# Performance work log

Hardware: AMD Instinct MI355X
Metric: run time of the kernel (lower is better)

Reference implementation:

```python
import jax, jax.numpy as jnp
import numpy as np

B, M, N, E = 64, 100, 6400, 102400   # graphs, nodes/graph, total nodes, edges
H, D, EMB, IMG, NC = 4, 512, 768, 1024, 2
HD = H * D
EPS = 1e-5


def _bn2(x, g, b, m, v):
    # BatchNorm1d eval mode on [B, C]
    return (x - m) / jnp.sqrt(v + EPS) * g + b


def _bn3(x, g, b, m, v):
    # BatchNorm1d eval mode on [B, C, L] -> channel dim is axis 1 (node index)
    return (x - m[None, :, None]) / jnp.sqrt(v + EPS)[None, :, None] * g[None, :, None] + b[None, :, None]


def _gat(feat, src, dst, W, al, ar, bias):
    # DGL GATConv (eval: feat_drop is identity). feat: [N, F_in]
    h = (feat @ W.T).reshape(-1, H, D)                 # [N, H, D]
    el = (h * al[None]).sum(-1)                         # [N, H]
    er = (h * ar[None]).sum(-1)                         # [N, H]
    e = jax.nn.leaky_relu(el[src] + er[dst], negative_slope=0.2)  # [E, H]
    mx = jax.ops.segment_max(e, dst, num_segments=N)
    a = jnp.exp(e - mx[dst])
    s = jax.ops.segment_sum(a, dst, num_segments=N)
    alpha = a / s[dst]                                  # edge softmax over incoming edges
    out = jax.ops.segment_sum(h[src] * alpha[:, :, None], dst, num_segments=N)  # [N, H, D]
    return out + bias.reshape(1, H, D)


def setup_inputs() -> dict:
    key = jax.random.key(0)
    ks = iter(jax.random.split(key, 80))
    n = lambda *s: jax.random.normal(next(ks), s, dtype=jnp.float32)

    def bn(c):
        return (1.0 + 0.1 * n(c), 0.1 * n(c), 0.1 * n(c),
                0.5 + jax.random.uniform(next(ks), (c,), dtype=jnp.float32))

    s = 0.02
    inp = {}
    inp['img_embedding'] = n(B, IMG)
    inp['func_text_embedding'] = n(B, EMB)
    inp['unix_emb'] = n(N, EMB)
    inp['pos_emb'] = jax.random.uniform(next(ks), (N, 4), dtype=jnp.float32)
    inp['src'] = jax.random.randint(next(ks), (E,), 0, N)
    inp['dst'] = jax.random.randint(next(ks), (E,), 0, N)
    inp['gat1_W'] = n(HD, EMB) * s; inp['gat1_al'] = n(H, D) * 0.1; inp['gat1_ar'] = n(H, D) * 0.1; inp['gat1_b'] = jnp.zeros(HD)
    inp['gat2_W'] = n(HD, HD) * s; inp['gat2_al'] = n(H, D) * 0.1; inp['gat2_ar'] = n(H, D) * 0.1; inp['gat2_b'] = jnp.zeros(HD)
    inp['fc_W'] = n(D, HD) * s; inp['fc_b'] = jnp.zeros(D)
    inp['hidden_W'] = n(8, D, D) * s; inp['hidden_b'] = jnp.zeros((8, D))
    inp['bn_text_g'], inp['bn_text_b'], inp['bn_text_m'], inp['bn_text_v'] = bn(EMB)
    inp['fc_text_W'] = n(D, EMB) * s; inp['fc_text_b'] = jnp.zeros(D)
    inp['swin_g'], inp['swin_b'], inp['swin_m'], inp['swin_v'] = bn(IMG)
    inp['swinfc_W'] = n(D, IMG) * s; inp['swinfc_b'] = jnp.zeros(D)
    inp['bngat_g'], inp['bngat_b'], inp['bngat_m'], inp['bngat_v'] = bn(M)
    inp['fc_gat_W'] = n(480, D) * s; inp['fc_gat_b'] = jnp.zeros(480)
    inp['bnbb_g'], inp['bnbb_b'], inp['bnbb_m'], inp['bnbb_v'] = bn(M)
    inp['fc_bbox_W'] = n(32, 4) * s; inp['fc_bbox_b'] = jnp.zeros(32)
    inp['fbn_g'], inp['fbn_b'], inp['fbn_m'], inp['fbn_v'] = bn(3 * D)
    inp['final_W'] = n(NC, 3 * D) * s; inp['final_b'] = jnp.zeros(NC)
    return inp


def reference(img_embedding, func_text_embedding, unix_emb, pos_emb, src, dst,
              gat1_W, gat1_al, gat1_ar, gat1_b, gat2_W, gat2_al, gat2_ar, gat2_b,
              fc_W, fc_b, hidden_W, hidden_b,
              bn_text_g, bn_text_b, bn_text_m, bn_text_v, fc_text_W, fc_text_b,
              swin_g, swin_b, swin_m, swin_v, swinfc_W, swinfc_b,
              bngat_g, bngat_b, bngat_m, bngat_v, fc_gat_W, fc_gat_b,
              bnbb_g, bnbb_b, bnbb_m, bnbb_v, fc_bbox_W, fc_bbox_b,
              fbn_g, fbn_b, fbn_m, fbn_v, final_W, final_b):
    # image branch
    x = jax.nn.elu(_bn2(img_embedding, swin_g, swin_b, swin_m, swin_v) @ swinfc_W.T + swinfc_b)
    # text branch
    ft = jax.nn.elu(_bn2(func_text_embedding, bn_text_g, bn_text_b, bn_text_m, bn_text_v) @ fc_text_W.T + fc_text_b)
    # graph branch: two stacked GATConv layers (dropout is identity in eval)
    h = _gat(unix_emb, src, dst, gat1_W, gat1_al, gat1_ar, gat1_b).reshape(N, HD)
    h = _gat(h, src, dst, gat2_W, gat2_al, gat2_ar, gat2_b).reshape(N, HD)
    h = jax.nn.elu(h @ fc_W.T + fc_b)
    for i in range(8):
        h = jax.nn.elu(h @ hidden_W[i].T + hidden_b[i])
    # unbatch + pad to max_node=100 -> pure reshape (all graphs have exactly M nodes)
    h_i = h.reshape(B, M, D)
    pos_i = pos_emb.reshape(B, M, 4)
    h_i = jax.nn.elu(_bn3(h_i, bngat_g, bngat_b, bngat_m, bngat_v) @ fc_gat_W.T + fc_gat_b)      # [B, M, 480]
    pos_i = jax.nn.elu(_bn3(pos_i, bnbb_g, bnbb_b, bnbb_m, bnbb_v) @ fc_bbox_W.T + fc_bbox_b)    # [B, M, 32]
    h_feature = jnp.concatenate([h_i, pos_i], axis=2).mean(axis=1)                                # [B, 512]
    all_feats = jnp.concatenate([x, h_feature, ft], axis=1)                                       # [B, 1536]
    return _bn2(all_feats, fbn_g, fbn_b, fbn_m, fbn_v) @ final_W.T + final_b
```

## Files before the change

kernel.cpp:

```cpp
#include <hip/hip_runtime.h>
#include <math.h>

#define Bg   64
#define Mg   100
#define Ng   6400
#define Eg   102400
#define Hh   4
#define Dd   512
#define HDd  2048
#define EMBd 768
#define IMGd 1024
#define EPSc 1e-5f

typedef __bf16 bf16x8 __attribute__((ext_vector_type(8)));
typedef float  f32x4  __attribute__((ext_vector_type(4)));
typedef unsigned short us8v __attribute__((ext_vector_type(8)));

__device__ __forceinline__ float eluf(float x) { return x > 0.f ? x : expm1f(x); }

__device__ __forceinline__ unsigned short f2bf(float x) {
    unsigned int u = __builtin_bit_cast(unsigned int, x);
    u += 0x7FFFu + ((u >> 16) & 1u);
    return (unsigned short)(u >> 16);
}
__device__ __forceinline__ float bf2f(unsigned short s) {
    return __builtin_bit_cast(float, ((unsigned int)s) << 16);
}

__device__ __forceinline__ void gld16(const void* g, void* l) {
    __builtin_amdgcn_global_load_lds(
        (const __attribute__((address_space(1))) void*)g,
        (__attribute__((address_space(3))) void*)l, 16, 0, 0);
}

__global__ __launch_bounds__(256)
void gemm_bf16(const unsigned short* __restrict__ A,
               const unsigned short* __restrict__ W,
               const float* __restrict__ bias, void* __restrict__ C,
               int M, int N, int K, int act, int outbf)
{
    __shared__ __align__(16) unsigned short As[128 * 32];
    __shared__ __align__(16) unsigned short Bs[128 * 32];
    const int tid  = threadIdx.x;
    const int lane = tid & 63, wid = tid >> 6;
    const int bm = blockIdx.y * 128, bn = blockIdx.x * 128;
    const int wm = (wid >> 1) * 64, wn = (wid & 1) * 64;
    const int lrow = lane >> 2;
    const int lcol = (lane & 3) << 3;

    f32x4 acc[4][4] = {};

    const int ra = wid * 32;
    const unsigned short* gA0 = A + (size_t)(bm + ra + lrow) * K + lcol;
    const unsigned short* gA1 = A + (size_t)(bm + ra + 16 + lrow) * K + lcol;
    int rb0 = bn + ra + lrow;       if (rb0 >= N) rb0 = N - 1;
    int rb1 = bn + ra + 16 + lrow;  if (rb1 >= N) rb1 = N - 1;
    const unsigned short* gB0 = W + (size_t)rb0 * K + lcol;
    const unsigned short* gB1 = W + (size_t)rb1 * K + lcol;
    unsigned short* lA0 = &As[(ra)      * 32];
    unsigned short* lA1 = &As[(ra + 16) * 32];
    unsigned short* lB0 = &Bs[(ra)      * 32];
    unsigned short* lB1 = &Bs[(ra + 16) * 32];

    const int frow = lane & 15;
    const int quad = (lane >> 4) << 3;

    for (int k0 = 0; k0 < K; k0 += 32) {
        gld16(gA0 + k0, lA0);
        gld16(gA1 + k0, lA1);
        gld16(gB0 + k0, lB0);
        gld16(gB1 + k0, lB1);
        __syncthreads();
        bf16x8 af[4], bfr[4];
#pragma unroll
        for (int i = 0; i < 4; ++i)
            af[i]  = *(const bf16x8*)&As[(wm + i * 16 + frow) * 32 + quad];
#pragma unroll
        for (int i = 0; i < 4; ++i)
            bfr[i] = *(const bf16x8*)&Bs[(wn + i * 16 + frow) * 32 + quad];
#pragma unroll
        for (int mi = 0; mi < 4; ++mi)
#pragma unroll
            for (int ni = 0; ni < 4; ++ni)
                acc[mi][ni] = __builtin_amdgcn_mfma_f32_16x16x32_bf16(
                    af[mi], bfr[ni], acc[mi][ni], 0, 0, 0);
        __syncthreads();
    }

    const int crow0 = bm + wm + ((lane >> 4) << 2);
    const int ccol0 = bn + wn + (lane & 15);
#pragma unroll
    for (int mi = 0; mi < 4; ++mi) {
#pragma unroll
        for (int ni = 0; ni < 4; ++ni) {
            int col = ccol0 + ni * 16;
            if (col >= N) continue;
            float bv = bias ? bias[col] : 0.f;
#pragma unroll
            for (int r = 0; r < 4; ++r) {
                int row = crow0 + mi * 16 + r;
                float v = acc[mi][ni][r] + bv;
                if (act) v = eluf(v);
                if (outbf) ((unsigned short*)C)[(size_t)row * N + col] = f2bf(v);
                else       ((float*)C)[(size_t)row * N + col] = v;
            }
        }
    }
}

__global__ __launch_bounds__(256)
void gemm_t64b(const unsigned short* __restrict__ A,
               const unsigned short* __restrict__ W,
               const float* __restrict__ bias, void* __restrict__ C,
               int M, int N, int K, int act, int outbf)
{
    __shared__ __align__(16) unsigned short As[2 * 64 * 32];
    __shared__ __align__(16) unsigned short Bs[2 * 64 * 32];
    const int tid  = threadIdx.x;
    const int lane = tid & 63, wid = tid >> 6;
    const int bm = blockIdx.y * 64, bn = blockIdx.x * 64;
    const int wm = (wid >> 1) * 32, wn = (wid & 1) * 32;
    const int lrow = lane >> 2;
    const int lcol = (lane & 3) << 3;

    f32x4 acc[2][2] = {};

    const int r0 = wid * 16;
    const unsigned short* gA = A + (size_t)(bm + r0 + lrow) * K + lcol;
    int rb = bn + r0 + lrow; if (rb >= N) rb = N - 1;
    const unsigned short* gB = W + (size_t)rb * K + lcol;
    unsigned short* lA0 = &As[r0 * 32];
    unsigned short* lA1 = &As[2048 + r0 * 32];
    unsigned short* lB0 = &Bs[r0 * 32];
    unsigned short* lB1 = &Bs[2048 + r0 * 32];

    const int frow = lane & 15;
    const int quad = (lane >> 4) << 3;

    for (int k0 = 0; k0 < K; k0 += 64) {
        gld16(gA + k0,      lA0);
        gld16(gA + k0 + 32, lA1);
        gld16(gB + k0,      lB0);
        gld16(gB + k0 + 32, lB1);
        __syncthreads();
#pragma unroll
        for (int ks = 0; ks < 2; ++ks) {
            bf16x8 af0 = *(const bf16x8*)&As[ks * 2048 + (wm + frow) * 32 + quad];
            bf16x8 af1 = *(const bf16x8*)&As[ks * 2048 + (wm + 16 + frow) * 32 + quad];
            bf16x8 bf0 = *(const bf16x8*)&Bs[ks * 2048 + (wn + frow) * 32 + quad];
            bf16x8 bf1 = *(const bf16x8*)&Bs[ks * 2048 + (wn + 16 + frow) * 32 + quad];
            acc[0][0] = __builtin_amdgcn_mfma_f32_16x16x32_bf16(af0, bf0, acc[0][0], 0, 0, 0);
            acc[0][1] = __builtin_amdgcn_mfma_f32_16x16x32_bf16(af0, bf1, acc[0][1], 0, 0, 0);
            acc[1][0] = __builtin_amdgcn_mfma_f32_16x16x32_bf16(af1, bf0, acc[1][0], 0, 0, 0);
            acc[1][1] = __builtin_amdgcn_mfma_f32_16x16x32_bf16(af1, bf1, acc[1][1], 0, 0, 0);
        }
        __syncthreads();
    }

    const int crow0 = bm + wm + ((lane >> 4) << 2);
    const int ccol0 = bn + wn + (lane & 15);
#pragma unroll
    for (int mi = 0; mi < 2; ++mi) {
#pragma unroll
        for (int ni = 0; ni < 2; ++ni) {
            int col = ccol0 + ni * 16;
            if (col >= N) continue;
            float bv = bias ? bias[col] : 0.f;
#pragma unroll
            for (int r = 0; r < 4; ++r) {
                int row = crow0 + mi * 16 + r;
                float v = acc[mi][ni][r] + bv;
                if (act) v = eluf(v);
                if (outbf) ((unsigned short*)C)[(size_t)row * N + col] = f2bf(v);
                else       ((float*)C)[(size_t)row * N + col] = v;
            }
        }
    }
}

__global__ __launch_bounds__(256)
void gemm_t64b_fcgat(const unsigned short* __restrict__ A,
                     const unsigned short* __restrict__ W,
                     const float* __restrict__ bfg, const float* __restrict__ wsum,
                     const float* __restrict__ bng, const float* __restrict__ bnb,
                     const float* __restrict__ bnm, const float* __restrict__ bnv,
                     unsigned short* __restrict__ Eout, int M, int N, int K)
{
    __shared__ __align__(16) unsigned short As[2 * 64 * 32];
    __shared__ __align__(16) unsigned short Bs[2 * 64 * 32];
    const int tid  = threadIdx.x;
    const int lane = tid & 63, wid = tid >> 6;
    const int bm = blockIdx.y * 64, bn = blockIdx.x * 64;
    const int wm = (wid >> 1) * 32, wn = (wid & 1) * 32;
    const int lrow = lane >> 2;
    const int lcol = (lane & 3) << 3;

    f32x4 acc[2][2] = {};

    const int r0 = wid * 16;
    const unsigned short* gA = A + (size_t)(bm + r0 + lrow) * K + lcol;
    int rb = bn + r0 + lrow; if (rb >= N) rb = N - 1;
    const unsigned short* gB = W + (size_t)rb * K + lcol;
    unsigned short* lA0 = &As[r0 * 32];
    unsigned short* lA1 = &As[2048 + r0 * 32];
    unsigned short* lB0 = &Bs[r0 * 32];
    unsigned short* lB1 = &Bs[2048 + r0 * 32];

    const int frow = lane & 15;
    const int quad = (lane >> 4) << 3;

    for (int k0 = 0; k0 < K; k0 += 64) {
        gld16(gA + k0,      lA0);
        gld16(gA + k0 + 32, lA1);
        gld16(gB + k0,      lB0);
        gld16(gB + k0 + 32, lB1);
        __syncthreads();
#pragma unroll
        for (int ks = 0; ks < 2; ++ks) {
            bf16x8 af0 = *(const bf16x8*)&As[ks * 2048 + (wm + frow) * 32 + quad];
            bf16x8 af1 = *(const bf16x8*)&As[ks * 2048 + (wm + 16 + frow) * 32 + quad];
            bf16x8 bf0 = *(const bf16x8*)&Bs[ks * 2048 + (wn + frow) * 32 + quad];
            bf16x8 bf1 = *(const bf16x8*)&Bs[ks * 2048 + (wn + 16 + frow) * 32 + quad];
            acc[0][0] = __builtin_amdgcn_mfma_f32_16x16x32_bf16(af0, bf0, acc[0][0], 0, 0, 0);
            acc[0][1] = __builtin_amdgcn_mfma_f32_16x16x32_bf16(af0, bf1, acc[0][1], 0, 0, 0);
            acc[1][0] = __builtin_amdgcn_mfma_f32_16x16x32_bf16(af1, bf0, acc[1][0], 0, 0, 0);
            acc[1][1] = __builtin_amdgcn_mfma_f32_16x16x32_bf16(af1, bf1, acc[1][1], 0, 0, 0);
        }
        __syncthreads();
    }

    const int crow0 = bm + wm + ((lane >> 4) << 2);
    const int ccol0 = bn + wn + (lane & 15);
#pragma unroll
    for (int mi = 0; mi < 2; ++mi) {
#pragma unroll
        for (int r = 0; r < 4; ++r) {
            int row = crow0 + mi * 16 + r;
            int p = row % Mg;
            float sc = rsqrtf(bnv[p] + EPSc) * bng[p];
            float sh = bnb[p] - bnm[p] * sc;
#pragma unroll
            for (int ni = 0; ni < 2; ++ni) {
                int col = ccol0 + ni * 16;
                if (col < N) {
                    float v = sc * acc[mi][ni][r] + sh * wsum[col] + bfg[col];
                    Eout[(size_t)row * N + col] = f2bf(eluf(v));
                }
            }
        }
    }
}

__global__ __launch_bounds__(256)
void wsum_kernel(const float* __restrict__ W, float* __restrict__ s)
{
    int row = (blockIdx.x << 2) + (threadIdx.x >> 6);
    int lane = threadIdx.x & 63;
    if (row >= 480) return;
    const float* p = W + (size_t)row * Dd;
    float a = 0.f;
    for (int k = lane; k < Dd; k += 64) a += p[k];
#pragma unroll
    for (int o = 32; o > 0; o >>= 1) a += __shfl_down(a, o, 64);
    if (lane == 0) s[row] = a;
}

__global__ __launch_bounds__(256)
void gemm_nt(const float* __restrict__ A, const float* __restrict__ W,
             const float* __restrict__ bias, float* __restrict__ C,
             int M, int N, int K, int act)
{
    __shared__ float As[16 * 68];
    __shared__ float Ws[16 * 68];
    const int tid = threadIdx.x;
    const int tx = tid & 15, ty = tid >> 4;
    const int bm = blockIdx.y * 64, bn = blockIdx.x * 64;
    const int lrow = tid >> 2;
    const int lk4  = (tid & 3) << 2;
    const int arow = bm + lrow;
    const int wrow = bn + lrow;
    const float* Aptr = A + (size_t)arow * K + lk4;
    const float* Wptr = W + (size_t)wrow * K + lk4;
    float acc[4][4] = {{0.f,0.f,0.f,0.f},{0.f,0.f,0.f,0.f},{0.f,0.f,0.f,0.f},{0.f,0.f,0.f,0.f}};

    for (int k0 = 0; k0 < K; k0 += 16) {
        float4 av = make_float4(0.f,0.f,0.f,0.f);
        float4 wv = make_float4(0.f,0.f,0.f,0.f);
        if (arow < M) av = *(const float4*)(Aptr + k0);
        if (wrow < N) wv = *(const float4*)(Wptr + k0);
        As[(lk4+0)*68 + lrow] = av.x;
        As[(lk4+1)*68 + lrow] = av.y;
        As[(lk4+2)*68 + lrow] = av.z;
        As[(lk4+3)*68 + lrow] = av.w;
        Ws[(lk4+0)*68 + lrow] = wv.x;
        Ws[(lk4+1)*68 + lrow] = wv.y;
        Ws[(lk4+2)*68 + lrow] = wv.z;
        Ws[(lk4+3)*68 + lrow] = wv.w;
        __syncthreads();
#pragma unroll
        for (int kk = 0; kk < 16; ++kk) {
            float4 a = *(const float4*)&As[kk*68 + (ty<<2)];
            float4 w = *(const float4*)&Ws[kk*68 + (tx<<2)];
            acc[0][0] += a.x*w.x; acc[0][1] += a.x*w.y; acc[0][2] += a.x*w.z; acc[0][3] += a.x*w.w;
            acc[1][0] += a.y*w.x; acc[1][1] += a.y*w.y; acc[1][2] += a.y*w.z; acc[1][3] += a.y*w.w;
            acc[2][0] += a.z*w.x; acc[2][1] += a.z*w.y; acc[2][2] += a.z*w.z; acc[2][3] += a.z*w.w;
            acc[3][0] += a.w*w.x; acc[3][1] += a.w*w.y; acc[3][2] += a.w*w.z; acc[3][3] += a.w*w.w;
        }
        __syncthreads();
    }

#pragma unroll
    for (int i = 0; i < 4; ++i) {
        int row = bm + (ty<<2) + i;
        int col = bn + (tx<<2);
        if (row < M && col < N) {
            float4 v;
            v.x = acc[i][0]; v.y = acc[i][1]; v.z = acc[i][2]; v.w = acc[i][3];
            if (bias) { v.x += bias[col]; v.y += bias[col+1]; v.z += bias[col+2]; v.w += bias[col+3]; }
            if (act == 1) { v.x = eluf(v.x); v.y = eluf(v.y); v.z = eluf(v.z); v.w = eluf(v.w); }
            *(float4*)(C + (size_t)row * N + col) = v;
        }
    }
}

struct CvtPack {
    const float* s[6];
    unsigned short* d[6];
    int n4[6];
};

__global__ void cvt_all(CvtPack p, int total4)
{
    int i = blockIdx.x * 256 + threadIdx.x;
    if (i >= total4) return;
#pragma unroll
    for (int k = 0; k < 6; ++k) {
        if (i < p.n4[k]) {
            float4 v = ((const float4*)p.s[k])[i];
            ushort4 o;
            o.x = f2bf(v.x); o.y = f2bf(v.y); o.z = f2bf(v.z); o.w = f2bf(v.w);
            ((ushort4*)p.d[k])[i] = o;
            return;
        }
        i -= p.n4[k];
    }
}

__global__ void bn_col(const float* __restrict__ x, const float* __restrict__ g,
                       const float* __restrict__ b, const float* __restrict__ m,
                       const float* __restrict__ v, float* __restrict__ y,
                       int rows, int cols)
{
    int i = blockIdx.x * 256 + threadIdx.x;
    if (i >= rows * cols) return;
    int c = i % cols;
    float inv = rsqrtf(v[c] + EPSc);
    y[i] = (x[i] - m[c]) * inv * g[c] + b[c];
}

__global__ void zero_i32(int* __restrict__ p, int n)
{
    int i = blockIdx.x * 256 + threadIdx.x;
    if (i < n) p[i] = 0;
}

__global__ void count_dst(const int* __restrict__ dst, int* __restrict__ counts, int E)
{
    int i = blockIdx.x * 256 + threadIdx.x;
    if (i < E) atomicAdd(&counts[dst[i]], 1);
}

__global__ __launch_bounds__(1024)
void scan_excl(const int* __restrict__ counts, int* __restrict__ offs,
               int* __restrict__ cursor, int n)
{
    const int T = 7;
    int tid = threadIdx.x;
    int base = tid * T;
    int v[T];
    int tot = 0;
#pragma unroll
    for (int j = 0; j < T; ++j) {
        int i = base + j;
        v[j] = (i < n) ? counts[i] : 0;
        tot += v[j];
    }
    int lane = tid & 63, w = tid >> 6;
    int incl = tot;
#pragma unroll
    for (int o = 1; o < 64; o <<= 1) {
        int t = __shfl_up(incl, o, 64);
        if (lane >= o) incl += t;
    }
    __shared__ int wtot[16];
    __shared__ int wbase[16];
    if (lane == 63) wtot[w] = incl;
    __syncthreads();
    if (tid == 0) {
        int s = 0;
        for (int i = 0; i < 16; ++i) { wbase[i] = s; s += wtot[i]; }
    }
    __syncthreads();
    int ex = wbase[w] + incl - tot;
#pragma unroll
    for (int j = 0; j < T; ++j) {
        int i = base + j;
        if (i < n) { offs[i] = ex; cursor[i] = ex; }
        ex += v[j];
    }
    if (tid == 1023) offs[n] = ex;
}

__global__ void scatter_edges(const int* __restrict__ dst, int* __restrict__ cursor,
                              int* __restrict__ eid, int E)
{
    int i = blockIdx.x * 256 + threadIdx.x;
    if (i < E) {
        int p = atomicAdd(&cursor[dst[i]], 1);
        eid[p] = i;
    }
}

__global__ __launch_bounds__(256)
void elr_kernel(const unsigned short* __restrict__ Hm, const float* __restrict__ al,
                const float* __restrict__ ar, float* __restrict__ el,
                float* __restrict__ er)
{
    int wid = threadIdx.x >> 6, lane = threadIdx.x & 63;
    int g = (blockIdx.x << 2) + wid;
    int n = g >> 2, h = g & 3;
    const unsigned short* hp = Hm + ((size_t)n << 11) + (h << 9) + (lane << 3);
    const float* alp = al + (h << 9) + (lane << 3);
    const float* arp = ar + (h << 9) + (lane << 3);
    ushort4 x0 = *(const ushort4*)hp;
    ushort4 x1 = *(const ushort4*)(hp + 4);
    float4 l0 = *(const float4*)alp, l1 = *(const float4*)(alp + 4);
    float4 r0 = *(const float4*)arp, r1 = *(const float4*)(arp + 4);
    float a0 = bf2f(x0.x), a1 = bf2f(x0.y), a2 = bf2f(x0.z), a3 = bf2f(x0.w);
    float a4 = bf2f(x1.x), a5 = bf2f(x1.y), a6 = bf2f(x1.z), a7 = bf2f(x1.w);
    float se = a0*l0.x + a1*l0.y + a2*l0.z + a3*l0.w + a4*l1.x + a5*l1.y + a6*l1.z + a7*l1.w;
    float sr = a0*r0.x + a1*r0.y + a2*r0.z + a3*r0.w + a4*r1.x + a5*r1.y + a6*r1.z + a7*r1.w;
#pragma unroll
    for (int o = 32; o > 0; o >>= 1) {
        se += __shfl_down(se, o, 64);
        sr += __shfl_down(sr, o, 64);
    }
    if (lane == 0) { el[g] = se; er[g] = sr; }
}

__global__ __launch_bounds__(256)
void gat_agg(const unsigned short* __restrict__ Hm, const float* __restrict__ el,
             const float* __restrict__ er, const int* __restrict__ src,
             const int* __restrict__ offs, const int* __restrict__ eid,
             const float* __restrict__ bias, unsigned short* __restrict__ out)
{
    int n = blockIdx.x;
    int tid = threadIdx.x;
    int beg = offs[n], end = offs[n + 1];
    int deg = end - beg;
    const int d0 = tid << 3;
    const int h  = tid >> 6;

    if (deg == 0) {
#pragma unroll
        for (int j = 0; j < 8; ++j)
            out[((size_t)n << 11) + d0 + j] = f2bf(bias[d0 + j]);
        return;
    }

    __shared__ float m_sh[4], s_sh[4], al_sh[4];
    __shared__ int   src_sh[128];
    __shared__ float logit_sh[512];
    __shared__ float w_sh[512];

    if (tid < 4) { m_sh[tid] = -INFINITY; s_sh[tid] = 0.f; }
    float acc[8] = {0.f,0.f,0.f,0.f,0.f,0.f,0.f,0.f};
    __syncthreads();

    for (int c0 = 0; c0 < deg; c0 += 128) {
        int cnt = min(128, deg - c0);
        for (int i = tid; i < cnt; i += 256) src_sh[i] = src[eid[beg + c0 + i]];
        __syncthreads();
        for (int idx = tid; idx < (cnt << 2); idx += 256) {
            int i = idx >> 2, hh = idx & 3;
            float x = el[(src_sh[i] << 2) + hh] + er[(n << 2) + hh];
            logit_sh[idx] = x > 0.f ? x : 0.2f * x;
        }
        __syncthreads();
        if (tid < 4) {
            float cm = -INFINITY;
            for (int i = 0; i < cnt; ++i) cm = fmaxf(cm, logit_sh[(i << 2) + tid]);
            float mn = fmaxf(m_sh[tid], cm);
            al_sh[tid] = expf(m_sh[tid] - mn);
            m_sh[tid] = mn;
        }
        __syncthreads();
        for (int idx = tid; idx < (cnt << 2); idx += 256)
            w_sh[idx] = expf(logit_sh[idx] - m_sh[idx & 3]);
        __syncthreads();
        if (tid < 4) {
            float cs = 0.f;
            for (int i = 0; i < cnt; ++i) cs += w_sh[(i << 2) + tid];
            s_sh[tid] = s_sh[tid] * al_sh[tid] + cs;
        }
        float rsc = al_sh[h];
#pragma unroll
        for (int j = 0; j < 8; ++j) acc[j] *= rsc;
        for (int i = 0; i < cnt; ++i) {
            const unsigned short* hp = Hm + ((size_t)src_sh[i] << 11) + d0;
            us8v a = *(const us8v*)hp;
            float w0 = w_sh[(i << 2) + h];
#pragma unroll
            for (int j = 0; j < 8; ++j) acc[j] += w0 * bf2f(a[j]);
        }
        __syncthreads();
    }

    float is = 1.f / s_sh[h];
#pragma unroll
    for (int j = 0; j < 8; ++j)
        out[((size_t)n << 11) + d0 + j] = f2bf(acc[j] * is + bias[d0 + j]);
}

__global__ __launch_bounds__(256)
void mean_kernel(const unsigned short* __restrict__ hg, const float* __restrict__ pos,
                 const float* __restrict__ bg, const float* __restrict__ bb_,
                 const float* __restrict__ bm_, const float* __restrict__ bv_,
                 const float* __restrict__ W, const float* __restrict__ bias,
                 float* __restrict__ hf)
{
    int bb = blockIdx.x;
    int tid = threadIdx.x;
    int c0 = tid, c1 = tid + 256;
    const unsigned short* hb = hg + (size_t)bb * Mg * 480;
    float s0 = 0.f, s1 = 0.f;
    for (int m = 0; m < Mg; ++m) {
        s0 += bf2f(hb[m * 480 + c0]);
        if (c1 < 480) s1 += bf2f(hb[m * 480 + c1]);
    }
    if (c1 >= 480) {
        int o = c1 - 480;
        float w0 = W[(o << 2) + 0], w1 = W[(o << 2) + 1];
        float w2 = W[(o << 2) + 2], w3 = W[(o << 2) + 3];
        float bo = bias[o];
        const float* pp = pos + (size_t)bb * Mg * 4;
        s1 = 0.f;
        for (int m = 0; m < Mg; ++m) {
            float sc = rsqrtf(bv_[m] + EPSc) * bg[m];
            float sh = bb_[m] - bm_[m] * sc;
            float a = bo + (pp[m*4+0]*sc+sh)*w0 + (pp[m*4+1]*sc+sh)*w1
                         + (pp[m*4+2]*sc+sh)*w2 + (pp[m*4+3]*sc+sh)*w3;
            s1 += eluf(a);
        }
    }
    hf[bb * 512 + c0] = s0 * 0.01f;
    hf[bb * 512 + c1] = s1 * 0.01f;
}

__global__ __launch_bounds__(256)
void final_kernel(const float* __restrict__ x, const float* __restrict__ hf,
                  const float* __restrict__ ft, const float* __restrict__ g,
                  const float* __restrict__ b, const float* __restrict__ m,
                  const float* __restrict__ v, const float* __restrict__ W,
                  const float* __restrict__ bias, float* __restrict__ out)
{
    int bb = blockIdx.x;
    int tid = threadIdx.x;
    float a0 = 0.f, a1 = 0.f;
    for (int c = tid; c < 1536; c += 256) {
        float xv = (c < 512) ? x[bb * 512 + c]
                 : (c < 1024) ? hf[bb * 512 + (c - 512)]
                              : ft[bb * 512 + (c - 1024)];
        float z = (xv - m[c]) * rsqrtf(v[c] + EPSc) * g[c] + b[c];
        a0 += z * W[c];
        a1 += z * W[1536 + c];
    }
    __shared__ float r0[256], r1[256];
    r0[tid] = a0; r1[tid] = a1;
    __syncthreads();
    for (int o = 128; o > 0; o >>= 1) {
        if (tid < o) { r0[tid] += r0[tid + o]; r1[tid] += r1[tid + o]; }
        __syncthreads();
    }
    if (tid == 0) {
        out[bb * 2 + 0] = r0[0] + bias[0];
        out[bb * 2 + 1] = r1[0] + bias[1];
    }
}

extern "C" void kernel_launch(void* const* d_in, const int* in_sizes, int n_in,
                              void* d_out, int out_size, void* d_ws, size_t ws_size,
                              hipStream_t stream)
{
    (void)in_sizes; (void)n_in; (void)out_size; (void)ws_size;

    const float* img   = (const float*)d_in[0];
    const float* ftxt  = (const float*)d_in[1];
    const float* unixe = (const float*)d_in[2];
    const float* pos   = (const float*)d_in[3];
    const int*   src   = (const int*)  d_in[4];
    const int*   dst   = (const int*)  d_in[5];
    const float* g1W   = (const float*)d_in[6];
    const float* g1al  = (const float*)d_in[7];
    const float* g1ar  = (const float*)d_in[8];
    const float* g1b   = (const float*)d_in[9];
    const float* g2W   = (const float*)d_in[10];
    const float* g2al  = (const float*)d_in[11];
    const float* g2ar  = (const float*)d_in[12];
    const float* g2b   = (const float*)d_in[13];
    const float* fcW   = (const float*)d_in[14];
    const float* fcb   = (const float*)d_in[15];
    const float* hidW  = (const float*)d_in[16];
    const float* hidb  = (const float*)d_in[17];
    const float* btg   = (const float*)d_in[18];
    const float* btb   = (const float*)d_in[19];
    const float* btm   = (const float*)d_in[20];
    const float* btv   = (const float*)d_in[21];
    const float* ftW   = (const float*)d_in[22];
    const float* ftbi  = (const float*)d_in[23];
    const float* swg   = (const float*)d_in[24];
    const float* swb   = (const float*)d_in[25];
    const float* swm   = (const float*)d_in[26];
    const float* swv   = (const float*)d_in[27];
    const float* swW   = (const float*)d_in[28];
    const float* swbi  = (const float*)d_in[29];
    const float* bgg   = (const float*)d_in[30];
    const float* bgb   = (const float*)d_in[31];
    const float* bgm   = (const float*)d_in[32];
    const float* bgv   = (const float*)d_in[33];
    const float* fgW   = (const float*)d_in[34];
    const float* fgb   = (const float*)d_in[35];
    const float* bbgp  = (const float*)d_in[36];
    const float* bbbp  = (const float*)d_in[37];
    const float* bbmp  = (const float*)d_in[38];
    const float* bbvp  = (const float*)d_in[39];
    const float* fbW   = (const float*)d_in[40];
    const float* fbb   = (const float*)d_in[41];
    const float* fng   = (const float*)d_in[42];
    const float* fnb   = (const float*)d_in[43];
    const float* fnm   = (const float*)d_in[44];
    const float* fnv   = (const float*)d_in[45];
    const float* fiW   = (const float*)d_in[46];
    const float* fib   = (const float*)d_in[47];
    float* out = (float*)d_out;

    char* p = (char*)d_ws;
    unsigned short* fA  = (unsigned short*)p; p += (size_t)Ng * HDd * 2;
    unsigned short* fB  = (unsigned short*)p; p += (size_t)Ng * HDd * 2;
    unsigned short* fC  = (unsigned short*)p; p += (size_t)Ng * Dd * 2;
    unsigned short* fD  = (unsigned short*)p; p += (size_t)Ng * Dd * 2;
    unsigned short* fE  = (unsigned short*)p; p += (size_t)Ng * 480 * 2;
    float*          el  = (float*)p;          p += (size_t)Ng * Hh * 4;
    float*          er  = (float*)p;          p += (size_t)Ng * Hh * 4;
    float*          xb  = (float*)p;          p += (size_t)Bg * Dd * 4;
    float*          ftb = (float*)p;          p += (size_t)Bg * Dd * 4;
    float*          hf  = (float*)p;          p += (size_t)Bg * Dd * 4;
    float*          ti  = (float*)p;          p += (size_t)Bg * IMGd * 4;
    float*          tt  = (float*)p;          p += (size_t)Bg * EMBd * 4;
    float*          wsm = (float*)p;          p += (size_t)480 * 4;
    unsigned short* ubf = (unsigned short*)p; p += (size_t)Ng * EMBd * 2;
    unsigned short* wg1 = (unsigned short*)p; p += (size_t)HDd * EMBd * 2;
    unsigned short* wg2 = (unsigned short*)p; p += (size_t)HDd * HDd * 2;
    unsigned short* wfc = (unsigned short*)p; p += (size_t)Dd * HDd * 2;
    unsigned short* whid= (unsigned short*)p; p += (size_t)8 * Dd * Dd * 2;
    unsigned short* wfg = (unsigned short*)p; p += (size_t)480 * Dd * 2;
    int* counts = (int*)p; p += (size_t)Ng * 4;
    int* offs   = (int*)p; p += (size_t)(Ng + 1) * 4 + 12;
    int* cursor = (int*)p; p += (size_t)Ng * 4;
    int* eid    = (int*)p; p += (size_t)Eg * 4;

    CvtPack cp;
    cp.s[0] = unixe; cp.d[0] = ubf;  cp.n4[0] = Ng * EMBd / 4;
    cp.s[1] = g1W;   cp.d[1] = wg1;  cp.n4[1] = HDd * EMBd / 4;
    cp.s[2] = g2W;   cp.d[2] = wg2;  cp.n4[2] = HDd * HDd / 4;
    cp.s[3] = fcW;   cp.d[3] = wfc;  cp.n4[3] = Dd * HDd / 4;
    cp.s[4] = hidW;  cp.d[4] = whid; cp.n4[4] = 8 * Dd * Dd / 4;
    cp.s[5] = fgW;   cp.d[5] = wfg;  cp.n4[5] = 480 * Dd / 4;
    int total4 = cp.n4[0] + cp.n4[1] + cp.n4[2] + cp.n4[3] + cp.n4[4] + cp.n4[5];
    cvt_all<<<(total4 + 255)/256, 256, 0, stream>>>(cp, total4);
    wsum_kernel<<<120, 256, 0, stream>>>(fgW, wsm);

    bn_col<<<(Bg*IMGd + 255)/256, 256, 0, stream>>>(img, swg, swb, swm, swv, ti, Bg, IMGd);
    gemm_nt<<<dim3(8, 1), 256, 0, stream>>>(ti, swW, swbi, xb, Bg, Dd, IMGd, 1);
    bn_col<<<(Bg*EMBd + 255)/256, 256, 0, stream>>>(ftxt, btg, btb, btm, btv, tt, Bg, EMBd);
    gemm_nt<<<dim3(8, 1), 256, 0, stream>>>(tt, ftW, ftbi, ftb, Bg, Dd, EMBd, 1);

    zero_i32<<<(Ng + 255)/256, 256, 0, stream>>>(counts, Ng);
    count_dst<<<(Eg + 255)/256, 256, 0, stream>>>(dst, counts, Eg);
    scan_excl<<<1, 1024, 0, stream>>>(counts, offs, cursor, Ng);
    scatter_edges<<<(Eg + 255)/256, 256, 0, stream>>>(dst, cursor, eid, Eg);

    gemm_bf16<<<dim3(HDd/128, Ng/128), 256, 0, stream>>>(ubf, wg1, nullptr, fA, Ng, HDd, EMBd, 0, 1);
    elr_kernel<<<Ng, 256, 0, stream>>>(fA, g1al, g1ar, el, er);
    gat_agg<<<Ng, 256, 0, stream>>>(fA, el, er, src, offs, eid, g1b, fB);

    gemm_bf16<<<dim3(HDd/128, Ng/128), 256, 0, stream>>>(fB, wg2, nullptr, fA, Ng, HDd, HDd, 0, 1);
    elr_kernel<<<Ng, 256, 0, stream>>>(fA, g2al, g2ar, el, er);
    gat_agg<<<Ng, 256, 0, stream>>>(fA, el, er, src, offs, eid, g2b, fB);

    gemm_t64b<<<dim3(Dd/64, Ng/64), 256, 0, stream>>>(fB, wfc, fcb, fC, Ng, Dd, HDd, 1, 1);

    unsigned short* cur = fC; unsigned short* nxt = fD;
    for (int i = 0; i < 8; ++i) {
        gemm_t64b<<<dim3(Dd/64, Ng/64), 256, 0, stream>>>(
            cur, whid + (size_t)i * Dd * Dd, hidb + (size_t)i * Dd, nxt, Ng, Dd, Dd, 1, 1);
        unsigned short* t = cur; cur = nxt; nxt = t;
    }

    gemm_t64b_fcgat<<<dim3(8, Ng/64), 256, 0, stream>>>(
        cur, wfg, fgb, wsm, bgg, bgb, bgm, bgv, fE, Ng, 480, Dd);

    mean_kernel<<<Bg, 256, 0, stream>>>(fE, pos, bbgp, bbbp, bbmp, bbvp, fbW, fbb, hf);

    final_kernel<<<Bg, 256, 0, stream>>>(xb, hf, ftb, fng, fnb, fnm, fnv, fiW, fib, out);
}
```

Baseline: 856.3 us.

## Double-buffer LDS in GEMMs, fuse BN into small GEMMs, prefetch GAT gathers

Converts the three bf16 MFMA GEMM kernels to double-buffered LDS, issuing the next K-tile's global-to-LDS loads before computing the current one. This replaces the load-sync-compute pattern and its two barriers per step with one barrier per iteration. It also folds the eval-mode batchnorm into the A-load of the small fp32 gemm_nt, removing the bn_col kernels and their temporary buffers. The GAT aggregation loop now prefetches the next neighbour's feature row to hide gather latency. Costs are doubled shared memory in the GEMMs, which may reduce occupancy, and extra registers in the aggregation loop.

```diff
diff --git a/kernel.cpp b/kernel.cpp
--- a/kernel.cpp
+++ b/kernel.cpp
@@ -39,8 +39,8 @@
                const float* __restrict__ bias, void* __restrict__ C,
                int M, int N, int K, int act, int outbf)
 {
-    __shared__ __align__(16) unsigned short As[128 * 32];
-    __shared__ __align__(16) unsigned short Bs[128 * 32];
+    __shared__ __align__(16) unsigned short As[2 * 128 * 32];
+    __shared__ __align__(16) unsigned short Bs[2 * 128 * 32];
     const int tid  = threadIdx.x;
     const int lane = tid & 63, wid = tid >> 6;
     const int bm = blockIdx.y * 128, bn = blockIdx.x * 128;
@@ -57,27 +57,35 @@
     int rb1 = bn + ra + 16 + lrow;  if (rb1 >= N) rb1 = N - 1;
     const unsigned short* gB0 = W + (size_t)rb0 * K + lcol;
     const unsigned short* gB1 = W + (size_t)rb1 * K + lcol;
-    unsigned short* lA0 = &As[(ra)      * 32];
-    unsigned short* lA1 = &As[(ra + 16) * 32];
-    unsigned short* lB0 = &Bs[(ra)      * 32];
-    unsigned short* lB1 = &Bs[(ra + 16) * 32];
 
     const int frow = lane & 15;
     const int quad = (lane >> 4) << 3;
-
-    for (int k0 = 0; k0 < K; k0 += 32) {
-        gld16(gA0 + k0, lA0);
-        gld16(gA1 + k0, lA1);
-        gld16(gB0 + k0, lB0);
-        gld16(gB1 + k0, lB1);
-        __syncthreads();
+    const int iters = K >> 5;
+
+    gld16(gA0, &As[(ra)      * 32]);
+    gld16(gA1, &As[(ra + 16) * 32]);
+    gld16(gB0, &Bs[(ra)      * 32]);
+    gld16(gB1, &Bs[(ra + 16) * 32]);
+    __syncthreads();
+
+    int cur = 0;
+    for (int it = 0; it < iters; ++it) {
+        if (it + 1 < iters) {
+            int k1 = (it + 1) << 5;
+            int nb = (cur ^ 1) * 4096;
+            gld16(gA0 + k1, &As[nb + (ra)      * 32]);
+            gld16(gA1 + k1, &As[nb + (ra + 16) * 32]);
+            gld16(gB0 + k1, &Bs[nb + (ra)      * 32]);
+            gld16(gB1 + k1, &Bs[nb + (ra + 16) * 32]);
+        }
+        int cb = cur * 4096;
         bf16x8 af[4], bfr[4];
 #pragma unroll
         for (int i = 0; i < 4; ++i)
-            af[i]  = *(const bf16x8*)&As[(wm + i * 16 + frow) * 32 + quad];
+            af[i]  = *(const bf16x8*)&As[cb + (wm + i * 16 + frow) * 32 + quad];
 #pragma unroll
         for (int i = 0; i < 4; ++i)
-            bfr[i] = *(const bf16x8*)&Bs[(wn + i * 16 + frow) * 32 + quad];
+            bfr[i] = *(const bf16x8*)&Bs[cb + (wn + i * 16 + frow) * 32 + quad];
 #pragma unroll
         for (int mi = 0; mi < 4; ++mi)
 #pragma unroll
@@ -85,6 +93,7 @@
                 acc[mi][ni] = __builtin_amdgcn_mfma_f32_16x16x32_bf16(
                     af[mi], bfr[ni], acc[mi][ni], 0, 0, 0);
         __syncthreads();
+        cur ^= 1;
     }
 
     const int crow0 = bm + wm + ((lane >> 4) << 2);
@@ -114,8 +123,8 @@
                const float* __restrict__ bias, void* __restrict__ C,
                int M, int N, int K, int act, int outbf)
 {
-    __shared__ __align__(16) unsigned short As[2 * 64 * 32];
-    __shared__ __align__(16) unsigned short Bs[2 * 64 * 32];
+    __shared__ __align__(16) unsigned short As[2 * 2 * 64 * 32];
+    __shared__ __align__(16) unsigned short Bs[2 * 2 * 64 * 32];
     const int tid  = threadIdx.x;
     const int lane = tid & 63, wid = tid >> 6;
     const int bm = blockIdx.y * 64, bn = blockIdx.x * 64;
@@ -129,32 +138,41 @@
     const unsigned short* gA = A + (size_t)(bm + r0 + lrow) * K + lcol;
     int rb = bn + r0 + lrow; if (rb >= N) rb = N - 1;
     const unsigned short* gB = W + (size_t)rb * K + lcol;
-    unsigned short* lA0 = &As[r0 * 32];
-    unsigned short* lA1 = &As[2048 + r0 * 32];
-    unsigned short* lB0 = &Bs[r0 * 32];
-    unsigned short* lB1 = &Bs[2048 + r0 * 32];
 
     const int frow = lane & 15;
     const int quad = (lane >> 4) << 3;
-
-    for (int k0 = 0; k0 < K; k0 += 64) {
-        gld16(gA + k0,      lA0);
-        gld16(gA + k0 + 32, lA1);
-        gld16(gB + k0,      lB0);
-        gld16(gB + k0 + 32, lB1);
-        __syncthreads();
+    const int iters = K >> 6;
+
+    gld16(gA,      &As[r0 * 32]);
+    gld16(gA + 32, &As[2048 + r0 * 32]);
+    gld16(gB,      &Bs[r0 * 32]);
+    gld16(gB + 32, &Bs[2048 + r0 * 32]);
+    __syncthreads();
+
+    int cur = 0;
+    for (int it = 0; it < iters; ++it) {
+        if (it + 1 < iters) {
+            int k1 = (it + 1) << 6;
+            int nb = (cur ^ 1) * 4096;
+            gld16(gA + k1,      &As[nb + r0 * 32]);
+            gld16(gA + k1 + 32, &As[nb + 2048 + r0 * 32]);
+            gld16(gB + k1,      &Bs[nb + r0 * 32]);
+            gld16(gB + k1 + 32, &Bs[nb + 2048 + r0 * 32]);
+        }
+        int cb = cur * 4096;
 #pragma unroll
         for (int ks = 0; ks < 2; ++ks) {
-            bf16x8 af0 = *(const bf16x8*)&As[ks * 2048 + (wm + frow) * 32 + quad];
-            bf16x8 af1 = *(const bf16x8*)&As[ks * 2048 + (wm + 16 + frow) * 32 + quad];
-            bf16x8 bf0 = *(const bf16x8*)&Bs[ks * 2048 + (wn + frow) * 32 + quad];
-            bf16x8 bf1 = *(const bf16x8*)&Bs[ks * 2048 + (wn + 16 + frow) * 32 + quad];
+            bf16x8 af0 = *(const bf16x8*)&As[cb + ks * 2048 + (wm + frow) * 32 + quad];
+            bf16x8 af1 = *(const bf16x8*)&As[cb + ks * 2048 + (wm + 16 + frow) * 32 + quad];
+            bf16x8 bf0 = *(const bf16x8*)&Bs[cb + ks * 2048 + (wn + frow) * 32 + quad];
+            bf16x8 bf1 = *(const bf16x8*)&Bs[cb + ks * 2048 + (wn + 16 + frow) * 32 + quad];
             acc[0][0] = __builtin_amdgcn_mfma_f32_16x16x32_bf16(af0, bf0, acc[0][0], 0, 0, 0);
             acc[0][1] = __builtin_amdgcn_mfma_f32_16x16x32_bf16(af0, bf1, acc[0][1], 0, 0, 0);
             acc[1][0] = __builtin_amdgcn_mfma_f32_16x16x32_bf16(af1, bf0, acc[1][0], 0, 0, 0);
             acc[1][1] = __builtin_amdgcn_mfma_f32_16x16x32_bf16(af1, bf1, acc[1][1], 0, 0, 0);
         }
         __syncthreads();
+        cur ^= 1;
     }
 
     const int crow0 = bm + wm + ((lane >> 4) << 2);
@@ -186,8 +204,8 @@
                      const float* __restrict__ bnm, const float* __restrict__ bnv,
                      unsigned short* __restrict__ Eout, int M, int N, int K)
 {
-    __shared__ __align__(16) unsigned short As[2 * 64 * 32];
-    __shared__ __align__(16) unsigned short Bs[2 * 64 * 32];
+    __shared__ __align__(16) unsigned short As[2 * 2 * 64 * 32];
+    __shared__ __align__(16) unsigned short Bs[2 * 2 * 64 * 32];
     const int tid  = threadIdx.x;
     const int lane = tid & 63, wid = tid >> 6;
     const int bm = blockIdx.y * 64, bn = blockIdx.x * 64;
@@ -201,32 +219,41 @@
     const unsigned short* gA = A + (size_t)(bm + r0 + lrow) * K + lcol;
     int rb = bn + r0 + lrow; if (rb >= N) rb = N - 1;
     const unsigned short* gB = W + (size_t)rb * K + lcol;
-    unsigned short* lA0 = &As[r0 * 32];
-    unsigned short* lA1 = &As[2048 + r0 * 32];
-    unsigned short* lB0 = &Bs[r0 * 32];
-    unsigned short* lB1 = &Bs[2048 + r0 * 32];
 
     const int frow = lane & 15;
     const int quad = (lane >> 4) << 3;
-
-    for (int k0 = 0; k0 < K; k0 += 64) {
-        gld16(gA + k0,      lA0);
-        gld16(gA + k0 + 32, lA1);
-        gld16(gB + k0,      lB0);
-        gld16(gB + k0 + 32, lB1);
-        __syncthreads();
+    const int iters = K >> 6;
+
+    gld16(gA,      &As[r0 * 32]);
+    gld16(gA + 32, &As[2048 + r0 * 32]);
+    gld16(gB,      &Bs[r0 * 32]);
+    gld16(gB + 32, &Bs[2048 + r0 * 32]);
+    __syncthreads();
+
+    int cur = 0;
+    for (int it = 0; it < iters; ++it) {
+        if (it + 1 < iters) {
+            int k1 = (it + 1) << 6;
+            int nb = (cur ^ 1) * 4096;
+            gld16(gA + k1,      &As[nb + r0 * 32]);
+            gld16(gA + k1 + 32, &As[nb + 2048 + r0 * 32]);
+            gld16(gB + k1,      &Bs[nb + r0 * 32]);
+            gld16(gB + k1 + 32, &Bs[nb + 2048 + r0 * 32]);
+        }
+        int cb = cur * 4096;
 #pragma unroll
         for (int ks = 0; ks < 2; ++ks) {
-            bf16x8 af0 = *(const bf16x8*)&As[ks * 2048 + (wm + frow) * 32 + quad];
-            bf16x8 af1 = *(const bf16x8*)&As[ks * 2048 + (wm + 16 + frow) * 32 + quad];
-            bf16x8 bf0 = *(const bf16x8*)&Bs[ks * 2048 + (wn + frow) * 32 + quad];
-            bf16x8 bf1 = *(const bf16x8*)&Bs[ks * 2048 + (wn + 16 + frow) * 32 + quad];
+            bf16x8 af0 = *(const bf16x8*)&As[cb + ks * 2048 + (wm + frow) * 32 + quad];
+            bf16x8 af1 = *(const bf16x8*)&As[cb + ks * 2048 + (wm + 16 + frow) * 32 + quad];
+            bf16x8 bf0 = *(const bf16x8*)&Bs[cb + ks * 2048 + (wn + frow) * 32 + quad];
+            bf16x8 bf1 = *(const bf16x8*)&Bs[cb + ks * 2048 + (wn + 16 + frow) * 32 + quad];
             acc[0][0] = __builtin_amdgcn_mfma_f32_16x16x32_bf16(af0, bf0, acc[0][0], 0, 0, 0);
             acc[0][1] = __builtin_amdgcn_mfma_f32_16x16x32_bf16(af0, bf1, acc[0][1], 0, 0, 0);
             acc[1][0] = __builtin_amdgcn_mfma_f32_16x16x32_bf16(af1, bf0, acc[1][0], 0, 0, 0);
             acc[1][1] = __builtin_amdgcn_mfma_f32_16x16x32_bf16(af1, bf1, acc[1][1], 0, 0, 0);
         }
         __syncthreads();
+        cur ^= 1;
     }
 
     const int crow0 = bm + wm + ((lane >> 4) << 2);
@@ -268,7 +295,9 @@
 __global__ __launch_bounds__(256)
 void gemm_nt(const float* __restrict__ A, const float* __restrict__ W,
              const float* __restrict__ bias, float* __restrict__ C,
-             int M, int N, int K, int act)
+             int M, int N, int K, int act,
+             const float* __restrict__ bng, const float* __restrict__ bnb,
+             const float* __restrict__ bnm, const float* __restrict__ bnv)
 {
     __shared__ float As[16 * 68];
     __shared__ float Ws[16 * 68];
@@ -288,6 +317,21 @@
         float4 wv = make_float4(0.f,0.f,0.f,0.f);
         if (arow < M) av = *(const float4*)(Aptr + k0);
         if (wrow < N) wv = *(const float4*)(Wptr + k0);
+        if (bng) {
+            int c = lk4 + k0;
+            float4 gg = *(const float4*)(bng + c);
+            float4 bb = *(const float4*)(bnb + c);
+            float4 mm = *(const float4*)(bnm + c);
+            float4 vv = *(const float4*)(bnv + c);
+            float s0 = rsqrtf(vv.x + EPSc) * gg.x;
+            float s1 = rsqrtf(vv.y + EPSc) * gg.y;
+            float s2 = rsqrtf(vv.z + EPSc) * gg.z;
+            float s3 = rsqrtf(vv.w + EPSc) * gg.w;
+            av.x = (av.x - mm.x) * s0 + bb.x;
+            av.y = (av.y - mm.y) * s1 + bb.y;
+            av.z = (av.z - mm.z) * s2 + bb.z;
+            av.w = (av.w - mm.w) * s3 + bb.w;
+        }
         As[(lk4+0)*68 + lrow] = av.x;
         As[(lk4+1)*68 + lrow] = av.y;
         As[(lk4+2)*68 + lrow] = av.z;
@@ -344,18 +388,6 @@
         }
         i -= p.n4[k];
     }
-}
-
-__global__ void bn_col(const float* __restrict__ x, const float* __restrict__ g,
-                       const float* __restrict__ b, const float* __restrict__ m,
-                       const float* __restrict__ v, float* __restrict__ y,
-                       int rows, int cols)
-{
-    int i = blockIdx.x * 256 + threadIdx.x;
-    if (i >= rows * cols) return;
-    int c = i % cols;
-    float inv = rsqrtf(v[c] + EPSc);
-    y[i] = (x[i] - m[c]) * inv * g[c] + b[c];
 }
 
 __global__ void zero_i32(int* __restrict__ p, int n)
@@ -506,12 +538,16 @@
         float rsc = al_sh[h];
 #pragma unroll
         for (int j = 0; j < 8; ++j) acc[j] *= rsc;
+
+        us8v a = *(const us8v*)(Hm + ((size_t)src_sh[0] << 11) + d0);
         for (int i = 0; i < cnt; ++i) {
-            const unsigned short* hp = Hm + ((size_t)src_sh[i] << 11) + d0;
-            us8v a = *(const us8v*)hp;
+            us8v a_next;
+            if (i + 1 < cnt)
+                a_next = *(const us8v*)(Hm + ((size_t)src_sh[i + 1] << 11) + d0);
             float w0 = w_sh[(i << 2) + h];
 #pragma unroll
             for (int j = 0; j < 8; ++j) acc[j] += w0 * bf2f(a[j]);
+            if (i + 1 < cnt) a = a_next;
         }
         __syncthreads();
     }
@@ -655,8 +691,6 @@
     float*          xb  = (float*)p;          p += (size_t)Bg * Dd * 4;
     float*          ftb = (float*)p;          p += (size_t)Bg * Dd * 4;
     float*          hf  = (float*)p;          p += (size_t)Bg * Dd * 4;
-    float*          ti  = (float*)p;          p += (size_t)Bg * IMGd * 4;
-    float*          tt  = (float*)p;          p += (size_t)Bg * EMBd * 4;
     float*          wsm = (float*)p;          p += (size_t)480 * 4;
     unsigned short* ubf = (unsigned short*)p; p += (size_t)Ng * EMBd * 2;
     unsigned short* wg1 = (unsigned short*)p; p += (size_t)HDd * EMBd * 2;
@@ -680,10 +714,10 @@
     cvt_all<<<(total4 + 255)/256, 256, 0, stream>>>(cp, total4);
     wsum_kernel<<<120, 256, 0, stream>>>(fgW, wsm);
 
-    bn_col<<<(Bg*IMGd + 255)/256, 256, 0, stream>>>(img, swg, swb, swm, swv, ti, Bg, IMGd);
-    gemm_nt<<<dim3(8, 1), 256, 0, stream>>>(ti, swW, swbi, xb, Bg, Dd, IMGd, 1);
-    bn_col<<<(Bg*EMBd + 255)/256, 256, 0, stream>>>(ftxt, btg, btb, btm, btv, tt, Bg, EMBd);
-    gemm_nt<<<dim3(8, 1), 256, 0, stream>>>(tt, ftW, ftbi, ftb, Bg, Dd, EMBd, 1);
+    gemm_nt<<<dim3(8, 1), 256, 0, stream>>>(img, swW, swbi, xb, Bg, Dd, IMGd, 1,
+                                            swg, swb, swm, swv);
+    gemm_nt<<<dim3(8, 1), 256, 0, stream>>>(ftxt, ftW, ftbi, ftb, Bg, Dd, EMBd, 1,
+                                            btg, btb, btm, btv);
 
     zero_i32<<<(Ng + 255)/256, 256, 0, stream>>>(counts, Ng);
     count_dst<<<(Eg + 255)/256, 256, 0, stream>>>(dst, counts, Eg);
```

Measured after the change: 869.3 us. Within noise of the previous version (+1.5%).
